# Kernel optimization log

Measured on AMD Instinct MI355X. Metric: run time of the kernel, lower is better.

The kernel has to match this reference:

```python
import jax, jax.numpy as jnp
import numpy as np
from jax import lax
import math

B, CH, BINS, CROP = 8, 2, 1024, 1024
NUM_BANDS = 4
FF = 2048
EPS = 1e-5
SCALE = 0.02  # weight init scale for numeric stability


def _inorm(x, g, b):
    # InstanceNorm2d: x [B, C, H, W], normalize over (H, W) per (B, C); biased var
    m = x.mean(axis=(2, 3), keepdims=True)
    v = x.var(axis=(2, 3), keepdims=True)
    return (x - m) / jnp.sqrt(v + EPS) * g[None, :, None, None] + b[None, :, None, None]


def _dwconv(x, k):
    # depthwise conv1d: x [B, bins, W], k [bins, 1, 3], padding=1, groups=bins
    return lax.conv_general_dilated(x, k, (1,), [(1, 1)],
                                    dimension_numbers=('NCH', 'OIH', 'NCH'),
                                    feature_group_count=x.shape[1])


def setup_inputs() -> dict:
    key = jax.random.key(0)
    ks = jax.random.split(key, 12)
    inp = {
        'x': jax.random.normal(ks[0], (B, CH, BINS, CROP), jnp.float32),
        'prev_qk': jax.random.normal(ks[1], (B, NUM_BANDS, CROP, CROP), jnp.float32),
        'g_in': jnp.ones((CROP,), jnp.float32),
        'b_in': jnp.zeros((CROP,), jnp.float32),
        'W_in': jax.random.normal(ks[2], (1, CH), jnp.float32) * SCALE,
        'bias_in': jnp.zeros((1,), jnp.float32),
        'g1': jnp.ones((CROP,), jnp.float32),
        'b1': jnp.zeros((CROP,), jnp.float32),
        'Wq': jax.random.normal(ks[3], (BINS, BINS), jnp.float32) * SCALE,
        'Wk': jax.random.normal(ks[4], (BINS, BINS), jnp.float32) * SCALE,
        'Wv': jax.random.normal(ks[5], (BINS, BINS), jnp.float32) * SCALE,
        'Wo': jax.random.normal(ks[6], (BINS, BINS), jnp.float32) * SCALE,
        'kq': jax.random.normal(ks[7], (BINS, 1, 3), jnp.float32) * SCALE,
        'kk': jax.random.normal(ks[8], (BINS, 1, 3), jnp.float32) * SCALE,
        'kv': jax.random.normal(ks[9], (BINS, 1, 3), jnp.float32) * SCALE,
        'pos_w': jax.random.normal(ks[10], (BINS // NUM_BANDS, CROP), jnp.float32) * SCALE,
        'g2': jnp.ones((CROP,), jnp.float32),
        'b2': jnp.zeros((CROP,), jnp.float32),
        'W_ff': jax.random.normal(ks[11], (1, 2), jnp.float32) * SCALE,
        'bias_ff': jnp.zeros((1,), jnp.float32),
        'W1': jax.random.normal(jax.random.fold_in(key, 100), (FF, BINS), jnp.float32) * SCALE,
        'W2': jax.random.normal(jax.random.fold_in(key, 101), (BINS, FF), jnp.float32) * SCALE,
    }
    return inp


def reference(x, prev_qk, g_in, b_in, W_in, bias_in, g1, b1, Wq, Wk, Wv, Wo,
              kq, kk, kv, pos_w, g2, b2, W_ff, bias_ff, W1, W2):
    b = x.shape[0]
    nb = NUM_BANDS
    hd = BINS // nb
    # in_norm + in_project: transposed layout [B, CROP, BINS, CH]
    xt = jnp.transpose(x, (0, 3, 2, 1))
    xt = _inorm(xt, g_in, b_in)
    xt = jnp.einsum('bwhc,oc->bwho', xt, W_in) + bias_in  # [B,CROP,BINS,1]
    x0 = jnp.transpose(xt, (0, 3, 2, 1))                  # [B,1,BINS,CROP]
    # norm1 + attention over frames (w == CROP, c == BINS)
    h = jnp.transpose(_inorm(jnp.transpose(x0, (0, 3, 2, 1)), g1, b1), (0, 3, 2, 1))
    a_in = jnp.transpose(h, (0, 3, 2, 1))[..., 0]         # [B, W, BINS]
    q = jnp.einsum('bwc,oc->bwo', a_in, Wq)
    q = jnp.transpose(_dwconv(jnp.transpose(q, (0, 2, 1)), kq), (0, 2, 1))
    k = jnp.einsum('bwc,oc->bwo', a_in, Wk)
    k = jnp.transpose(_dwconv(jnp.transpose(k, (0, 2, 1)), kk), (0, 2, 1))
    v = jnp.einsum('bwc,oc->bwo', a_in, Wv)
    v = jnp.transpose(_dwconv(jnp.transpose(v, (0, 2, 1)), kv), (0, 2, 1))
    q4 = jnp.transpose(q.reshape(b, CROP, nb, hd), (0, 2, 1, 3))   # [B,nb,W,hd]
    k4 = jnp.transpose(k.reshape(b, CROP, nb, hd), (0, 2, 3, 1))   # [B,nb,hd,W]
    v4 = jnp.transpose(v.reshape(b, CROP, nb, hd), (0, 2, 1, 3))   # [B,nb,W,hd]
    # relative-position bias via pad-and-shift
    p = jnp.matmul(q4, pos_w)                                      # [B,nb,W,CROP]
    p = jnp.pad(p, ((0, 0), (0, 0), (0, 0), (1, 0)))
    p = jnp.swapaxes(p, 2, 3)[:, :, 1:, :]                         # [B,nb,CROP,W]
    qk = (jnp.matmul(q4, k4) + p) / math.sqrt(BINS)
    qk = qk + prev_qk
    a = jax.nn.softmax(qk, axis=-1)
    o = jnp.transpose(jnp.matmul(a, v4), (0, 2, 1, 3)).reshape(b, CROP, BINS)
    o = jnp.einsum('bwc,oc->bwo', o, Wo)                           # [B,W,BINS]
    h4 = jnp.transpose(o[..., None], (0, 3, 2, 1))                 # [B,1,BINS,CROP]
    x1 = jnp.concatenate([x0, h4], axis=1)                         # [B,2,BINS,CROP]
    # norm2 + ff_project + squared-ReLU FFN
    hn = _inorm(jnp.transpose(x1, (0, 3, 2, 1)), g2, b2)           # [B,CROP,BINS,2]
    hn = jnp.einsum('bwhc,oc->bwho', hn, W_ff) + bias_ff           # [B,CROP,BINS,1]
    hn = jnp.transpose(hn, (0, 3, 2, 1))                           # [B,1,BINS,CROP]
    ht = jnp.swapaxes(hn, 2, 3)                                    # [B,1,CROP,BINS]
    ht = jnp.square(jax.nn.relu(jnp.einsum('bowc,fc->bowf', ht, W1)))
    ht = jnp.einsum('bowf,cf->bowc', ht, W2)
    hf = jnp.swapaxes(ht, 2, 3)                                    # [B,1,BINS,CROP]
    out = jnp.concatenate([x1, hf], axis=1)                        # [B,3,BINS,CROP]
    return out, qk
```

## Files before the change

### kernel.cpp

```cpp
#include <hip/hip_runtime.h>
#include <stdint.h>

#define DEVI __device__ __forceinline__

typedef __attribute__((ext_vector_type(8))) short bf16x8;
typedef __attribute__((ext_vector_type(4))) float f32x4;

#define B_    8
#define CROP_ 1024
#define BINS_ 1024
#define NB_   4
#define HD_   256
#define FF_   2048
#define EPSF  1e-5f
#define OUT0_ELEMS (8ull*3ull*1024ull*1024ull)
#define MBYTE (1024ull*1024ull)
#define M1ELEM (1024ll*1024ll)
#define SMCAP 8.0f

DEVI unsigned short f2bf(float f) {
  unsigned u = __builtin_bit_cast(unsigned, f);
  u += 0x7fffu + ((u >> 16) & 1u);
  return (unsigned short)(u >> 16);
}
DEVI float bf2f(unsigned short h) {
  unsigned u = ((unsigned)h) << 16;
  return __builtin_bit_cast(float, u);
}

DEVI void gload16(const unsigned short* g, unsigned short* l) {
  __builtin_amdgcn_global_load_lds(
      (const __attribute__((address_space(1))) unsigned int*)g,
      (__attribute__((address_space(3))) unsigned int*)l, 16, 0, 0);
}

__global__ __launch_bounds__(256) void k_conv_all(
    const float* __restrict__ Wq, const float* __restrict__ Wk,
    const float* __restrict__ Wv, const float* __restrict__ Wo,
    const float* __restrict__ W1, const float* __restrict__ W2,
    const float* __restrict__ pw,
    unsigned short* __restrict__ WQKVB, unsigned short* __restrict__ WOB,
    unsigned short* __restrict__ W1B, unsigned short* __restrict__ W2B,
    unsigned short* __restrict__ PWT) {
  long long i = (long long)blockIdx.x*256 + threadIdx.x;
  long long stride = (long long)gridDim.x*256;
  const long long total = 8*M1ELEM + (1 << 18);
  for (; i < total; i += stride) {
    if (i < 3*M1ELEM) {
      const float* s = i < M1ELEM ? Wq : (i < 2*M1ELEM ? Wk : Wv);
      WQKVB[i] = f2bf(s[i & (M1ELEM-1)]);
    } else if (i < 4*M1ELEM) { WOB[i-3*M1ELEM] = f2bf(Wo[i-3*M1ELEM]); }
    else if (i < 6*M1ELEM)   { W1B[i-4*M1ELEM] = f2bf(W1[i-4*M1ELEM]); }
    else if (i < 8*M1ELEM)   { W2B[i-6*M1ELEM] = f2bf(W2[i-6*M1ELEM]); }
    else {
      long long j = i - 8*M1ELEM;
      int w = (int)(j >> 8), d = (int)(j & 255);
      PWT[j] = f2bf(pw[d*1024 + w]);
    }
  }
}

__global__ __launch_bounds__(256) void k_instx0(const float* __restrict__ x,
    const float* __restrict__ g_in, const float* __restrict__ b_in,
    const float* __restrict__ W_in, const float* __restrict__ bias_in,
    float* __restrict__ outp, float* __restrict__ x0t) {
  int b = blockIdx.y, w0 = blockIdx.x*32;
  int t = threadIdx.x, wl = t & 31, p = t >> 5;
  const float* xb = x + (size_t)b*2*M1ELEM + w0 + wl;
  float s = 0.f, ss = 0.f;
  for (int i = p*256; i < p*256 + 256; ++i) {
    float v = xb[(size_t)i*CROP_];
    s += v; ss += v*v;
  }
  __shared__ float ls[8][32], lss[8][32];
  __shared__ float s_coef[32], s_add[32];
  ls[p][wl] = s; lss[p][wl] = ss;
  __syncthreads();
  float W0 = W_in[0], W1 = W_in[1], bi = bias_in[0];
  float sW = W0 + W1;
  if (t < 32) {
    float S = 0.f, SS = 0.f;
    for (int q = 0; q < 8; ++q) { S += ls[q][t]; SS += lss[q][t]; }
    float m = S*(1.f/2048.f);
    float var = SS*(1.f/2048.f) - m*m;
    float r = rsqrtf(var + EPSF);
    int w = w0 + t;
    float coef = r*g_in[w];
    s_coef[t] = coef;
    s_add[t] = b_in[w]*sW + bi - coef*m*sW;
  }
  __syncthreads();
  __shared__ float tile[32][33];
  int tx = wl, ty = p;
  float coef = s_coef[tx], add = s_add[tx];
  int w = w0 + tx;
  for (int h0 = 0; h0 < BINS_; h0 += 32) {
#pragma unroll
    for (int q = 0; q < 4; ++q) {
      int h = h0 + ty + q*8;
      size_t i0 = ((size_t)b*2*BINS_ + h)*CROP_ + w;
      float val = coef*(W0*x[i0] + W1*x[i0 + (size_t)M1ELEM]) + add;
      outp[(((size_t)b*3)*BINS_ + h)*CROP_ + w] = val;
      tile[ty + q*8][tx] = val;
    }
    __syncthreads();
#pragma unroll
    for (int q = 0; q < 4; ++q)
      x0t[((size_t)b*CROP_ + w0 + ty + q*8)*BINS_ + h0 + tx] = tile[tx][ty + q*8];
    __syncthreads();
  }
}

__global__ __launch_bounds__(256) void k_norm1(const float* __restrict__ x0t,
    const float* __restrict__ g1, const float* __restrict__ b1,
    unsigned short* __restrict__ ain) {
  int r = blockIdx.x;
  int w = r & (CROP_ - 1);
  int t = threadIdx.x;
  const float* row = x0t + (size_t)r*BINS_;
  float v[4], s = 0.f, ss = 0.f;
  for (int q = 0; q < 4; ++q) { v[q] = row[t + q*256]; s += v[q]; ss += v[q]*v[q]; }
  for (int off = 32; off; off >>= 1) { s += __shfl_xor(s, off); ss += __shfl_xor(ss, off); }
  __shared__ float red[8];
  int wv = t >> 6;
  if ((t & 63) == 0) { red[wv] = s; red[4 + wv] = ss; }
  __syncthreads();
  s = red[0] + red[1] + red[2] + red[3];
  ss = red[4] + red[5] + red[6] + red[7];
  float m = s*(1.f/1024.f);
  float var = ss*(1.f/1024.f) - m*m;
  float rs = rsqrtf(var + EPSF);
  float g = g1[w], bb = b1[w];
  for (int q = 0; q < 4; ++q)
    ain[(size_t)r*BINS_ + t + q*256] = f2bf((v[q] - m)*rs*g + bb);
}

__global__ __launch_bounds__(256) void k_norm2(const float* __restrict__ x0t,
    const float* __restrict__ o2,
    const float* __restrict__ g2, const float* __restrict__ b2,
    const float* __restrict__ W_ff, const float* __restrict__ bias_ff,
    unsigned short* __restrict__ hn) {
  int r = blockIdx.x;
  int w = r & (CROP_ - 1);
  int t = threadIdx.x;
  const float* ra = x0t + (size_t)r*BINS_;
  const float* rb = o2 + (size_t)r*BINS_;
  float va[4], vb[4], s = 0.f, ss = 0.f;
  for (int q = 0; q < 4; ++q) {
    va[q] = ra[t + q*256]; vb[q] = rb[t + q*256];
    s += va[q] + vb[q]; ss += va[q]*va[q] + vb[q]*vb[q];
  }
  for (int off = 32; off; off >>= 1) { s += __shfl_xor(s, off); ss += __shfl_xor(ss, off); }
  __shared__ float red[8];
  int wv = t >> 6;
  if ((t & 63) == 0) { red[wv] = s; red[4 + wv] = ss; }
  __syncthreads();
  s = red[0] + red[1] + red[2] + red[3];
  ss = red[4] + red[5] + red[6] + red[7];
  float m = s*(1.f/2048.f);
  float var = ss*(1.f/2048.f) - m*m;
  float rs = rsqrtf(var + EPSF);
  float W0 = W_ff[0], W1f = W_ff[1];
  float gg = g2[w]*rs;
  float add = b2[w]*(W0 + W1f) + bias_ff[0];
  for (int q = 0; q < 4; ++q)
    hn[(size_t)r*BINS_ + t + q*256] = f2bf(gg*(W0*(va[q] - m) + W1f*(vb[q] - m)) + add);
}

__global__ __launch_bounds__(256) void k_dwconv(const unsigned short* __restrict__ qkvb,
    const float* __restrict__ kq, const float* __restrict__ kk2,
    unsigned short* __restrict__ qkvc) {
  int w = blockIdx.x, b = blockIdx.y, which = blockIdx.z;
  int t = threadIdx.x;
  const float* kw = which == 0 ? kq : kk2;
  const unsigned short* r0 = qkvb + (size_t)which*8*M1ELEM + ((size_t)b*CROP_ + w)*BINS_;
  unsigned short* d0 = qkvc + (size_t)which*8*M1ELEM + ((size_t)b*CROP_ + w)*BINS_;
  for (int q = 0; q < 4; ++q) {
    int c = t + q*256;
    float k0 = kw[c*3], k1 = kw[c*3 + 1], k2 = kw[c*3 + 2];
    float acc = bf2f(r0[c]) * k1;
    if (w > 0)        acc += bf2f(r0[c - BINS_]) * k0;
    if (w < CROP_-1)  acc += bf2f(r0[c + BINS_]) * k2;
    d0[c] = f2bf(acc);
  }
}

__global__ __launch_bounds__(256) void k_dwconv_trV(const unsigned short* __restrict__ vb,
    const float* __restrict__ kv, unsigned short* __restrict__ vct) {
  int b = blockIdx.z;
  int w0 = blockIdx.x*32, c0 = blockIdx.y*32;
  int tx = threadIdx.x, ty = threadIdx.y;
  __shared__ unsigned short tile[34][33];
  const unsigned short* S = vb + (size_t)b*M1ELEM;
#pragma unroll
  for (int q = 0; q < 4; ++q) {
    int wl = ty + q*8;
    tile[wl + 1][tx] = S[(size_t)(w0 + wl)*BINS_ + c0 + tx];
  }
  if (ty == 0) tile[0][tx]  = (w0 > 0)          ? S[(size_t)(w0 - 1)*BINS_ + c0 + tx] : (unsigned short)0;
  if (ty == 1) tile[33][tx] = (w0 + 32 < CROP_) ? S[(size_t)(w0 + 32)*BINS_ + c0 + tx] : (unsigned short)0;
  __syncthreads();
  unsigned short* D = vct + (size_t)b*M1ELEM;
#pragma unroll
  for (int q = 0; q < 4; ++q) {
    int cl = ty + q*8;
    int c = c0 + cl;
    float k0 = kv[c*3], k1 = kv[c*3 + 1], k2 = kv[c*3 + 2];
    float val = k0*bf2f(tile[tx][cl]) + k1*bf2f(tile[tx + 1][cl]) + k2*bf2f(tile[tx + 2][cl]);
    D[(size_t)c*CROP_ + w0 + tx] = f2bf(val);
  }
}

#define BUFB 49152

template<int AC, int BC, int ABY>
DEVI void stage_gen(const unsigned short* Ab, int lda, const unsigned short* Bb, int ldb,
                    int k0, unsigned short* buf, int t, int wv) {
  int trow = t >> 3;
  int colel = ((t & 7) ^ (trow & 7)) << 3;
  unsigned short* lbase = buf + wv*512;
  const unsigned short* ga = Ab + (size_t)trow*lda + k0 + colel;
#pragma unroll
  for (int c = 0; c < AC; ++c)
    gload16(ga + (size_t)(c*64)*lda, lbase + c*4096);
  const unsigned short* gb = Bb + (size_t)trow*ldb + k0 + colel;
  unsigned short* lbb = buf + ABY/2 + wv*512;
#pragma unroll
  for (int c = 0; c < BC; ++c)
    gload16(gb + (size_t)(c*64)*ldb, lbb + c*4096);
}

template<int MODE>
__global__ __launch_bounds__(512) void k_gemm3(
    const unsigned short* __restrict__ A, int lda,
    const unsigned short* __restrict__ Bt, int ldb,
    void* __restrict__ C, int ldc, int K, float* __restrict__ C2, int ch)
{
  __shared__ __align__(16) unsigned short lds[3*24576];
  const unsigned short* Ab = A + (size_t)blockIdx.x*256*lda;
  const unsigned short* Bb = Bt + (size_t)blockIdx.y*128*ldb;
  const int t = threadIdx.x;
  const int wv = t >> 6, ln = t & 63;
  const int wm = wv >> 1, wn = wv & 1;
  const int lr = ln & 15, lk = ln >> 4;
  const int sx = (lr & 7) << 4;
  const int NT = K >> 6;
  stage_gen<4,2,32768>(Ab, lda, Bb, ldb, 0,   lds,           t, wv);
  stage_gen<4,2,32768>(Ab, lda, Bb, ldb, 64,  lds + 24576,   t, wv);
  stage_gen<4,2,32768>(Ab, lda, Bb, ldb, 128, lds + 49152,   t, wv);
  asm volatile("s_waitcnt vmcnt(12)" ::: "memory");
  __builtin_amdgcn_s_barrier();

  f32x4 acc[4][4] = {};
  for (int kt = 0; kt < NT; ++kt) {
    const int cur = kt % 3;
    const char* bufc = (const char*)lds + cur*BUFB;
    bf16x8 af[2][4], bf[2][4];
#pragma unroll
    for (int kk = 0; kk < 2; ++kk) {
#pragma unroll
      for (int mi = 0; mi < 4; ++mi) {
        int row = wm*64 + mi*16 + lr;
        af[kk][mi] = *(const bf16x8*)(bufc + ((row*128 + kk*64 + lk*16) ^ sx));
      }
#pragma unroll
      for (int ni = 0; ni < 4; ++ni) {
        int row = wn*64 + ni*16 + lr;
        bf[kk][ni] = *(const bf16x8*)(bufc + 32768 + ((row*128 + kk*64 + lk*16) ^ sx));
      }
    }
    asm volatile("s_waitcnt lgkmcnt(0)" ::: "memory");
    __builtin_amdgcn_s_barrier();
    if (kt + 3 < NT)
      stage_gen<4,2,32768>(Ab, lda, Bb, ldb, (kt+3)*64, (unsigned short*)((char*)lds + cur*BUFB), t, wv);
    __builtin_amdgcn_s_setprio(1);
#pragma unroll
    for (int kk = 0; kk < 2; ++kk)
#pragma unroll
      for (int mi = 0; mi < 4; ++mi)
#pragma unroll
        for (int ni = 0; ni < 4; ++ni)
          acc[mi][ni] = __builtin_amdgcn_mfma_f32_16x16x32_bf16(af[kk][mi], bf[kk][ni], acc[mi][ni], 0, 0, 0);
    __builtin_amdgcn_s_setprio(0);
    if (kt + 1 < NT) {
      int rem = (NT-1 < kt+3 ? NT-1 : kt+3) - (kt+1);
      if (rem >= 2)      asm volatile("s_waitcnt vmcnt(12)" ::: "memory");
      else if (rem == 1) asm volatile("s_waitcnt vmcnt(6)"  ::: "memory");
      else               asm volatile("s_waitcnt vmcnt(0)"  ::: "memory");
      __builtin_amdgcn_s_barrier();
    }
  }

  if (MODE != 3) {
    const int row0 = blockIdx.x*256 + wm*64 + lk*4;
    const int col0 = blockIdx.y*128 + wn*64 + lr;
#pragma unroll
    for (int mi = 0; mi < 4; ++mi)
#pragma unroll
      for (int ni = 0; ni < 4; ++ni)
#pragma unroll
        for (int j = 0; j < 4; ++j) {
          int row = row0 + mi*16 + j;
          int col = col0 + ni*16;
          float v = acc[mi][ni][j];
          if (MODE == 0 || MODE == 4) {
            ((float*)C)[(size_t)row*ldc + col] = v;
          } else if (MODE == 2) {
            float rr = fmaxf(v, 0.f);
            ((unsigned short*)C)[(size_t)row*ldc + col] = f2bf(rr*rr);
          } else if (MODE == 5) {
            ((unsigned short*)C)[(size_t)(col >> 10)*8*M1ELEM + (size_t)row*1024 + (col & 1023)] = f2bf(v);
          }
        }
  }
  if (MODE == 3 || MODE == 4) {
    __syncthreads();
    float* ldsT = (float*)lds + wv*4160;
#pragma unroll
    for (int mi = 0; mi < 4; ++mi)
#pragma unroll
      for (int ni = 0; ni < 4; ++ni)
#pragma unroll
        for (int j = 0; j < 4; ++j)
          ldsT[(ni*16 + lr)*65 + mi*16 + lk*4 + j] = acc[mi][ni][j];
    asm volatile("s_waitcnt lgkmcnt(0)" ::: "memory");
    int l16 = ln & 15, csub = ln >> 4;
    int b = blockIdx.x >> 2;
    int wbase = ((blockIdx.x & 3) << 8) + wm*64 + l16*4;
    float* outc = C2 + (((size_t)b*3 + ch)*BINS_)*CROP_;
#pragma unroll
    for (int cb = 0; cb < 16; ++cb) {
      int cl = cb*4 + csub;
      float4 v4;
      v4.x = ldsT[cl*65 + l16*4 + 0];
      v4.y = ldsT[cl*65 + l16*4 + 1];
      v4.z = ldsT[cl*65 + l16*4 + 2];
      v4.w = ldsT[cl*65 + l16*4 + 3];
      *(float4*)&outc[(size_t)(blockIdx.y*128 + wn*64 + cl)*CROP_ + wbase] = v4;
    }
  }
}

DEVI void stage_qk(const unsigned short* qc_b, const unsigned short* kc_b,
                   const unsigned short* pwt, int bx, int by, int k0,
                   unsigned short* buf, int t, int wv) {
  int trow = t >> 3;
  int colel = ((t & 7) ^ (trow & 7)) << 3;
  unsigned short* lbase = buf + wv*512;
  if (k0 < 256) {
    const unsigned short* ga = qc_b + (size_t)(bx*256 + trow)*BINS_ + k0 + colel;
#pragma unroll
    for (int c = 0; c < 4; ++c)
      gload16(ga + (size_t)(c*64)*BINS_, lbase + c*4096);
  } else {
    const unsigned short* ga = pwt + (size_t)(bx*256 + trow)*HD_ + (k0 - 256) + colel;
#pragma unroll
    for (int c = 0; c < 4; ++c)
      gload16(ga + (size_t)(c*64)*HD_, lbase + c*4096);
  }
  const unsigned short* gbsrc = (k0 < 256) ? kc_b : qc_b;
  int kb = (k0 < 256) ? k0 : k0 - 256;
  const unsigned short* gb = gbsrc + (size_t)(by*128 + trow)*BINS_ + kb + colel;
  unsigned short* lbb = buf + 16384 + wv*512;
#pragma unroll
  for (int c = 0; c < 2; ++c)
    gload16(gb + (size_t)(c*64)*BINS_, lbb + c*4096);
}

__global__ __launch_bounds__(512) void k_qkpos2(
    const unsigned short* __restrict__ qc, const unsigned short* __restrict__ kc,
    const unsigned short* __restrict__ pwt,
    const float* __restrict__ prev, float* __restrict__ qkout,
    unsigned short* __restrict__ Pbuf, float* __restrict__ Lg)
{
  __shared__ __align__(16) unsigned short lds[3*24576];
  const int z = blockIdx.z, b = z >> 2, n = z & 3;
  const size_t bandoff = (size_t)b*CROP_*BINS_ + (size_t)n*HD_;
  const unsigned short* qc_b = qc + bandoff;
  const unsigned short* kc_b = kc + bandoff;
  const int bx = blockIdx.x, by = blockIdx.y;
  const int t = threadIdx.x;
  const int wv = t >> 6, ln = t & 63;
  const int wm = wv >> 1, wn = wv & 1;
  const int lr = ln & 15, lk = ln >> 4;
  const int sx = (lr & 7) << 4;
  const int NT = 8;
  stage_qk(qc_b, kc_b, pwt, bx, by, 0,   lds,         t, wv);
  stage_qk(qc_b, kc_b, pwt, bx, by, 64,  lds + 24576, t, wv);
  stage_qk(qc_b, kc_b, pwt, bx, by, 128, lds + 49152, t, wv);
  asm volatile("s_waitcnt vmcnt(12)" ::: "memory");
  __builtin_amdgcn_s_barrier();

  f32x4 acc[4][4] = {};
  for (int kt = 0; kt < NT; ++kt) {
    const int cur = kt % 3;
    const char* bufc = (const char*)lds + cur*BUFB;
    bf16x8 af[2][4], bf[2][4];
#pragma unroll
    for (int kk = 0; kk < 2; ++kk) {
#pragma unroll
      for (int mi = 0; mi < 4; ++mi) {
        int row = wm*64 + mi*16 + lr;
        af[kk][mi] = *(const bf16x8*)(bufc + ((row*128 + kk*64 + lk*16) ^ sx));
      }
#pragma unroll
      for (int ni = 0; ni < 4; ++ni) {
        int row = wn*64 + ni*16 + lr;
        bf[kk][ni] = *(const bf16x8*)(bufc + 32768 + ((row*128 + kk*64 + lk*16) ^ sx));
      }
    }
    asm volatile("s_waitcnt lgkmcnt(0)" ::: "memory");
    __builtin_amdgcn_s_barrier();
    if (kt + 3 < NT)
      stage_qk(qc_b, kc_b, pwt, bx, by, (kt+3)*64, (unsigned short*)((char*)lds + cur*BUFB), t, wv);
    __builtin_amdgcn_s_setprio(1);
#pragma unroll
    for (int kk = 0; kk < 2; ++kk)
#pragma unroll
      for (int mi = 0; mi < 4; ++mi)
#pragma unroll
        for (int ni = 0; ni < 4; ++ni)
          acc[mi][ni] = __builtin_amdgcn_mfma_f32_16x16x32_bf16(af[kk][mi], bf[kk][ni], acc[mi][ni], 0, 0, 0);
    __builtin_amdgcn_s_setprio(0);
    if (kt + 1 < NT) {
      int rem = (NT-1 < kt+3 ? NT-1 : kt+3) - (kt+1);
      if (rem >= 2)      asm volatile("s_waitcnt vmcnt(12)" ::: "memory");
      else if (rem == 1) asm volatile("s_waitcnt vmcnt(6)"  ::: "memory");
      else               asm volatile("s_waitcnt vmcnt(0)"  ::: "memory");
      __builtin_amdgcn_s_barrier();
    }
  }

  const float* pz = prev + (size_t)z*M1ELEM;
  float* oz = qkout + (size_t)z*M1ELEM;
  unsigned short* Pz = Pbuf + (size_t)z*M1ELEM;
  const int row0g = bx*256;
  const int col0 = by*128 + wn*64 + lr;
  float* slf = (float*)lds;
  const int rbase = wm*64 + lk*4;
#pragma unroll
  for (int mi = 0; mi < 4; ++mi) {
    float psum[4] = {0.f, 0.f, 0.f, 0.f};
#pragma unroll
    for (int ni = 0; ni < 4; ++ni)
#pragma unroll
      for (int j = 0; j < 4; ++j) {
        size_t idx = (size_t)(row0g + rbase + mi*16 + j)*CROP_ + col0 + ni*16;
        float val = acc[mi][ni][j]*0.03125f + pz[idx];
        oz[idx] = val;
        float p = __expf(val - SMCAP);
        Pz[idx] = f2bf(p);
        psum[j] += p;
      }
#pragma unroll
    for (int off = 1; off < 16; off <<= 1)
#pragma unroll
      for (int j = 0; j < 4; ++j) psum[j] += __shfl_xor(psum[j], off);
    if (lr == 0)
#pragma unroll
      for (int j = 0; j < 4; ++j) slf[wn*256 + rbase + mi*16 + j] = psum[j];
  }
  __syncthreads();
  if (t < 256) {
    size_t si = ((size_t)z*CROP_ + row0g + t)*8 + by;
    Lg[si] = slf[t] + slf[256 + t];
  }
}

__global__ __launch_bounds__(512) void k_pv3(
    const unsigned short* __restrict__ P, const float* __restrict__ Lg,
    const unsigned short* __restrict__ vct, unsigned short* __restrict__ ob)
{
  __shared__ __align__(16) unsigned short lds[3*24576];
  __shared__ float s_il[128];
  const int z = blockIdx.y, b = z >> 2, band = z & 3;
  const int bx = blockIdx.x;
  const unsigned short* Ab = P + (size_t)z*M1ELEM + (size_t)bx*128*CROP_;
  const unsigned short* Bb = vct + ((size_t)b*CROP_ + band*HD_)*CROP_;
  const int t = threadIdx.x;
  const int wv = t >> 6, ln = t & 63;
  const int wm = wv >> 2, wn = wv & 3;
  const int lr = ln & 15, lk = ln >> 4;
  const int sx = (lr & 7) << 4;
  const int NT = 16;
  if (t < 128) {
    size_t rg = (size_t)z*CROP_ + bx*128 + t;
    float l = 0.f;
#pragma unroll
    for (int cb = 0; cb < 8; ++cb) l += Lg[rg*8 + cb];
    s_il[t] = 1.f / l;
  }
  stage_gen<2,4,16384>(Ab, CROP_, Bb, CROP_, 0,   lds,         t, wv);
  stage_gen<2,4,16384>(Ab, CROP_, Bb, CROP_, 64,  lds + 24576, t, wv);
  stage_gen<2,4,16384>(Ab, CROP_, Bb, CROP_, 128, lds + 49152, t, wv);
  asm volatile("s_waitcnt vmcnt(12) lgkmcnt(0)" ::: "memory");
  __builtin_amdgcn_s_barrier();

  f32x4 acc[4][4] = {};
  for (int kt = 0; kt < NT; ++kt) {
    const int cur = kt % 3;
    const char* bufc = (const char*)lds + cur*BUFB;
    bf16x8 af[2][4], bf[2][4];
#pragma unroll
    for (int kk = 0; kk < 2; ++kk) {
#pragma unroll
      for (int mi = 0; mi < 4; ++mi) {
        int row = wm*64 + mi*16 + lr;
        af[kk][mi] = *(const bf16x8*)(bufc + ((row*128 + kk*64 + lk*16) ^ sx));
      }
#pragma unroll
      for (int ni = 0; ni < 4; ++ni) {
        int row = wn*64 + ni*16 + lr;
        bf[kk][ni] = *(const bf16x8*)(bufc + 16384 + ((row*128 + kk*64 + lk*16) ^ sx));
      }
    }
    asm volatile("s_waitcnt lgkmcnt(0)" ::: "memory");
    __builtin_amdgcn_s_barrier();
    if (kt + 3 < NT)
      stage_gen<2,4,16384>(Ab, CROP_, Bb, CROP_, (kt+3)*64, (unsigned short*)((char*)lds + cur*BUFB), t, wv);
    __builtin_amdgcn_s_setprio(1);
#pragma unroll
    for (int kk = 0; kk < 2; ++kk)
#pragma unroll
      for (int mi = 0; mi < 4; ++mi)
#pragma unroll
        for (int ni = 0; ni < 4; ++ni)
          acc[mi][ni] = __builtin_amdgcn_mfma_f32_16x16x32_bf16(af[kk][mi], bf[kk][ni], acc[mi][ni], 0, 0, 0);
    __builtin_amdgcn_s_setprio(0);
    if (kt + 1 < NT) {
      int rem = (NT-1 < kt+3 ? NT-1 : kt+3) - (kt+1);
      if (rem >= 2)      asm volatile("s_waitcnt vmcnt(12)" ::: "memory");
      else if (rem == 1) asm volatile("s_waitcnt vmcnt(6)"  ::: "memory");
      else               asm volatile("s_waitcnt vmcnt(0)"  ::: "memory");
      __builtin_amdgcn_s_barrier();
    }
  }
#pragma unroll
  for (int mi = 0; mi < 4; ++mi)
#pragma unroll
    for (int j = 0; j < 4; ++j) {
      int rl = wm*64 + mi*16 + lk*4 + j;
      float il = s_il[rl];
#pragma unroll
      for (int ni = 0; ni < 4; ++ni) {
        int col = band*HD_ + wn*64 + ni*16 + lr;
        ob[((size_t)b*CROP_ + bx*128 + rl)*BINS_ + col] = f2bf(acc[mi][ni][j]*il);
      }
    }
}

extern "C" void kernel_launch(void* const* d_in, const int* in_sizes, int n_in,
                              void* d_out, int out_size, void* d_ws, size_t ws_size,
                              hipStream_t stream) {
  (void)in_sizes; (void)n_in; (void)out_size; (void)ws_size;
  const float* x       = (const float*)d_in[0];
  const float* prev_qk = (const float*)d_in[1];
  const float* g_in    = (const float*)d_in[2];
  const float* b_in    = (const float*)d_in[3];
  const float* W_in    = (const float*)d_in[4];
  const float* bias_in = (const float*)d_in[5];
  const float* g1      = (const float*)d_in[6];
  const float* b1      = (const float*)d_in[7];
  const float* Wq      = (const float*)d_in[8];
  const float* Wk      = (const float*)d_in[9];
  const float* Wv      = (const float*)d_in[10];
  const float* Wo      = (const float*)d_in[11];
  const float* kq      = (const float*)d_in[12];
  const float* kk      = (const float*)d_in[13];
  const float* kv      = (const float*)d_in[14];
  const float* pos_w   = (const float*)d_in[15];
  const float* g2      = (const float*)d_in[16];
  const float* b2      = (const float*)d_in[17];
  const float* W_ff    = (const float*)d_in[18];
  const float* bias_ff = (const float*)d_in[19];
  const float* W1      = (const float*)d_in[20];
  const float* W2      = (const float*)d_in[21];

  char* ws = (char*)d_ws;
  unsigned short* WQKVB = (unsigned short*)(ws + 0*MBYTE);
  unsigned short* WOB   = (unsigned short*)(ws + 6*MBYTE);
  unsigned short* W1B   = (unsigned short*)(ws + 8*MBYTE);
  unsigned short* W2B   = (unsigned short*)(ws + 12*MBYTE);
  unsigned short* PWT   = (unsigned short*)(ws + 16*MBYTE);
  float*          Lg    = (float*)(ws + 17*MBYTE);
  float*          X0T   = (float*)(ws + 20*MBYTE);
  unsigned short* AIN   = (unsigned short*)(ws + 52*MBYTE);
  unsigned short* QKVB  = (unsigned short*)(ws + 68*MBYTE);
  unsigned short* PBUF  = (unsigned short*)(ws + 52*MBYTE);
  unsigned short* QKVC  = (unsigned short*)(ws + 116*MBYTE);
  float*          O2    = (float*)(ws + 116*MBYTE);
  unsigned short* OB    = (unsigned short*)(ws + 148*MBYTE);
  unsigned short* VCT   = (unsigned short*)(ws + 164*MBYTE);
  unsigned short* HN    = (unsigned short*)(ws + 52*MBYTE);
  unsigned short* HT    = (unsigned short*)(ws + 20*MBYTE);

  float* outp  = (float*)d_out;
  float* qkout = outp + OUT0_ELEMS;

  dim3 blk256(256, 1, 1);
  dim3 blk512(512, 1, 1);
  dim3 blk32x8(32, 8, 1);

  k_conv_all<<<8448, blk256, 0, stream>>>(Wq, Wk, Wv, Wo, W1, W2, pos_w,
                                          WQKVB, WOB, W1B, W2B, PWT);
  k_instx0<<<dim3(32, 8, 1), blk256, 0, stream>>>(x, g_in, b_in, W_in, bias_in, outp, X0T);
  k_norm1<<<8192, blk256, 0, stream>>>(X0T, g1, b1, AIN);
  k_gemm3<5><<<dim3(32, 24, 1), blk512, 0, stream>>>(AIN, 1024, WQKVB, 1024, QKVB, 0, 1024, nullptr, 0);
  k_dwconv<<<dim3(1024, 8, 2), blk256, 0, stream>>>(QKVB, kq, kk, QKVC);
  k_dwconv_trV<<<dim3(32, 32, 8), blk32x8, 0, stream>>>(QKVB + (size_t)2*8*M1ELEM, kv, VCT);
  k_qkpos2<<<dim3(4, 8, 32), blk512, 0, stream>>>(QKVC, QKVC + (size_t)8*M1ELEM, PWT,
                                                  prev_qk, qkout, PBUF, Lg);
  k_pv3<<<dim3(8, 32, 1), blk512, 0, stream>>>(PBUF, Lg, VCT, OB);
  k_gemm3<4><<<dim3(32, 8, 1), blk512, 0, stream>>>(OB, 1024, WOB, 1024, O2, 1024, 1024, outp, 1);
  k_norm2<<<8192, blk256, 0, stream>>>(X0T, O2, g2, b2, W_ff, bias_ff, HN);
  k_gemm3<2><<<dim3(32, 16, 1), blk512, 0, stream>>>(HN, 1024, W1B, 1024, HT, 2048, 1024, nullptr, 0);
  k_gemm3<3><<<dim3(32, 8, 1), blk512, 0, stream>>>(HT, 2048, W2B, 2048, nullptr, 1024, 2048, outp, 2);
}
```

Before: 462.8 us.

## Split LDS fragment loads to overlap MFMA and add XCD-aware block swizzle

The GEMM inner loop now loads the first k-half of the A/B fragments, waits only for those, and issues their MFMAs while the second-half LDS reads are still in flight. The barrier and the next global-to-LDS prefetch are moved between the two MFMA halves. Separately, every GEMM kernel remaps its flat block index so that consecutive tiles land on the same XCD, which is meant to improve L2 reuse of shared A/B rows. This adds sched_barriers and index arithmetic, and the relaxed lgkmcnt wait relies on LDS reads completing in issue order.

```diff
diff --git a/kernel.cpp b/kernel.cpp
--- a/kernel.cpp
+++ b/kernel.cpp
@@ -32,6 +32,16 @@
   __builtin_amdgcn_global_load_lds(
       (const __attribute__((address_space(1))) unsigned int*)g,
       (__attribute__((address_space(3))) unsigned int*)l, 16, 0, 0);
+}
+
+DEVI void xcdswz(int& bx, int& by, int& bz) {
+  int gx = gridDim.x, gy = gridDim.y;
+  int nwg = gx*gy*gridDim.z;
+  int flat = blockIdx.x + gx*(blockIdx.y + gy*blockIdx.z);
+  int s = (flat & 7)*(nwg >> 3) + (flat >> 3);
+  bx = s % gx; s /= gx;
+  by = s % gy;
+  bz = s / gy;
 }
 
 __global__ __launch_bounds__(256) void k_conv_all(
@@ -230,6 +240,57 @@
     gload16(gb + (size_t)(c*64)*ldb, lbb + c*4096);
 }
 
+#define RING_BODY(BOFF, ...)                                                           \
+    bf16x8 af[2][4], bf[2][4];                                                         \
+    _Pragma("unroll")                                                                  \
+    for (int mi = 0; mi < 4; ++mi) {                                                   \
+      int row = wm*64 + mi*16 + lr;                                                    \
+      af[0][mi] = *(const bf16x8*)(bufc + ((row*128 + lk*16) ^ sx));                   \
+    }                                                                                  \
+    _Pragma("unroll")                                                                  \
+    for (int ni = 0; ni < 4; ++ni) {                                                   \
+      int row = wn*64 + ni*16 + lr;                                                    \
+      bf[0][ni] = *(const bf16x8*)(bufc + BOFF + ((row*128 + lk*16) ^ sx));            \
+    }                                                                                  \
+    __builtin_amdgcn_sched_barrier(0);                                                 \
+    _Pragma("unroll")                                                                  \
+    for (int mi = 0; mi < 4; ++mi) {                                                   \
+      int row = wm*64 + mi*16 + lr;                                                    \
+      af[1][mi] = *(const bf16x8*)(bufc + ((row*128 + 64 + lk*16) ^ sx));              \
+    }                                                                                  \
+    _Pragma("unroll")                                                                  \
+    for (int ni = 0; ni < 4; ++ni) {                                                   \
+      int row = wn*64 + ni*16 + lr;                                                    \
+      bf[1][ni] = *(const bf16x8*)(bufc + BOFF + ((row*128 + 64 + lk*16) ^ sx));       \
+    }                                                                                  \
+    asm volatile("s_waitcnt lgkmcnt(8)" ::: "memory");                                 \
+    __builtin_amdgcn_sched_barrier(0);                                                 \
+    __builtin_amdgcn_s_setprio(1);                                                     \
+    _Pragma("unroll")                                                                  \
+    for (int mi = 0; mi < 4; ++mi)                                                     \
+      _Pragma("unroll")                                                                \
+      for (int ni = 0; ni < 4; ++ni)                                                   \
+        acc[mi][ni] = __builtin_amdgcn_mfma_f32_16x16x32_bf16(af[0][mi], bf[0][ni], acc[mi][ni], 0, 0, 0); \
+    __builtin_amdgcn_s_setprio(0);                                                     \
+    __builtin_amdgcn_sched_barrier(0);                                                 \
+    asm volatile("s_waitcnt lgkmcnt(0)" ::: "memory");                                 \
+    __builtin_amdgcn_s_barrier();                                                      \
+    __VA_ARGS__;                                                                       \
+    __builtin_amdgcn_s_setprio(1);                                                     \
+    _Pragma("unroll")                                                                  \
+    for (int mi = 0; mi < 4; ++mi)                                                     \
+      _Pragma("unroll")                                                                \
+      for (int ni = 0; ni < 4; ++ni)                                                   \
+        acc[mi][ni] = __builtin_amdgcn_mfma_f32_16x16x32_bf16(af[1][mi], bf[1][ni], acc[mi][ni], 0, 0, 0); \
+    __builtin_amdgcn_s_setprio(0);                                                     \
+    if (kt + 1 < NT) {                                                                 \
+      int rem = (NT-1 < kt+3 ? NT-1 : kt+3) - (kt+1);                                  \
+      if (rem >= 2)      asm volatile("s_waitcnt vmcnt(12)" ::: "memory");             \
+      else if (rem == 1) asm volatile("s_waitcnt vmcnt(6)"  ::: "memory");             \
+      else               asm volatile("s_waitcnt vmcnt(0)"  ::: "memory");             \
+      __builtin_amdgcn_s_barrier();                                                    \
+    }
+
 template<int MODE>
 __global__ __launch_bounds__(512) void k_gemm3(
     const unsigned short* __restrict__ A, int lda,
@@ -237,8 +298,11 @@
     void* __restrict__ C, int ldc, int K, float* __restrict__ C2, int ch)
 {
   __shared__ __align__(16) unsigned short lds[3*24576];
-  const unsigned short* Ab = A + (size_t)blockIdx.x*256*lda;
-  const unsigned short* Bb = Bt + (size_t)blockIdx.y*128*ldb;
+  int bxs, bys, bzs;
+  xcdswz(bxs, bys, bzs);
+  (void)bzs;
+  const unsigned short* Ab = A + (size_t)bxs*256*lda;
+  const unsigned short* Bb = Bt + (size_t)bys*128*ldb;
   const int t = threadIdx.x;
   const int wv = t >> 6, ln = t & 63;
   const int wm = wv >> 1, wn = wv & 1;
@@ -255,45 +319,14 @@
   for (int kt = 0; kt < NT; ++kt) {
     const int cur = kt % 3;
     const char* bufc = (const char*)lds + cur*BUFB;
-    bf16x8 af[2][4], bf[2][4];
-#pragma unroll
-    for (int kk = 0; kk < 2; ++kk) {
-#pragma unroll
-      for (int mi = 0; mi < 4; ++mi) {
-        int row = wm*64 + mi*16 + lr;
-        af[kk][mi] = *(const bf16x8*)(bufc + ((row*128 + kk*64 + lk*16) ^ sx));
-      }
-#pragma unroll
-      for (int ni = 0; ni < 4; ++ni) {
-        int row = wn*64 + ni*16 + lr;
-        bf[kk][ni] = *(const bf16x8*)(bufc + 32768 + ((row*128 + kk*64 + lk*16) ^ sx));
-      }
-    }
-    asm volatile("s_waitcnt lgkmcnt(0)" ::: "memory");
-    __builtin_amdgcn_s_barrier();
-    if (kt + 3 < NT)
-      stage_gen<4,2,32768>(Ab, lda, Bb, ldb, (kt+3)*64, (unsigned short*)((char*)lds + cur*BUFB), t, wv);
-    __builtin_amdgcn_s_setprio(1);
-#pragma unroll
-    for (int kk = 0; kk < 2; ++kk)
-#pragma unroll
-      for (int mi = 0; mi < 4; ++mi)
-#pragma unroll
-        for (int ni = 0; ni < 4; ++ni)
-          acc[mi][ni] = __builtin_amdgcn_mfma_f32_16x16x32_bf16(af[kk][mi], bf[kk][ni], acc[mi][ni], 0, 0, 0);
-    __builtin_amdgcn_s_setprio(0);
-    if (kt + 1 < NT) {
-      int rem = (NT-1 < kt+3 ? NT-1 : kt+3) - (kt+1);
-      if (rem >= 2)      asm volatile("s_waitcnt vmcnt(12)" ::: "memory");
-      else if (rem == 1) asm volatile("s_waitcnt vmcnt(6)"  ::: "memory");
-      else               asm volatile("s_waitcnt vmcnt(0)"  ::: "memory");
-      __builtin_amdgcn_s_barrier();
-    }
+    RING_BODY(32768,
+      if (kt + 3 < NT) stage_gen<4,2,32768>(Ab, lda, Bb, ldb, (kt+3)*64,
+                                            (unsigned short*)((char*)lds + cur*BUFB), t, wv))
   }
 
   if (MODE != 3) {
-    const int row0 = blockIdx.x*256 + wm*64 + lk*4;
-    const int col0 = blockIdx.y*128 + wn*64 + lr;
+    const int row0 = bxs*256 + wm*64 + lk*4;
+    const int col0 = bys*128 + wn*64 + lr;
 #pragma unroll
     for (int mi = 0; mi < 4; ++mi)
 #pragma unroll
@@ -325,8 +358,8 @@
           ldsT[(ni*16 + lr)*65 + mi*16 + lk*4 + j] = acc[mi][ni][j];
     asm volatile("s_waitcnt lgkmcnt(0)" ::: "memory");
     int l16 = ln & 15, csub = ln >> 4;
-    int b = blockIdx.x >> 2;
-    int wbase = ((blockIdx.x & 3) << 8) + wm*64 + l16*4;
+    int b = bxs >> 2;
+    int wbase = ((bxs & 3) << 8) + wm*64 + l16*4;
     float* outc = C2 + (((size_t)b*3 + ch)*BINS_)*CROP_;
 #pragma unroll
     for (int cb = 0; cb < 16; ++cb) {
@@ -336,7 +369,7 @@
       v4.y = ldsT[cl*65 + l16*4 + 1];
       v4.z = ldsT[cl*65 + l16*4 + 2];
       v4.w = ldsT[cl*65 + l16*4 + 3];
-      *(float4*)&outc[(size_t)(blockIdx.y*128 + wn*64 + cl)*CROP_ + wbase] = v4;
+      *(float4*)&outc[(size_t)(bys*128 + wn*64 + cl)*CROP_ + wbase] = v4;
     }
   }
 }
@@ -374,11 +407,12 @@
     unsigned short* __restrict__ Pbuf, float* __restrict__ Lg)
 {
   __shared__ __align__(16) unsigned short lds[3*24576];
-  const int z = blockIdx.z, b = z >> 2, n = z & 3;
+  int bx, by, z;
+  xcdswz(bx, by, z);
+  const int b = z >> 2, n = z & 3;
   const size_t bandoff = (size_t)b*CROP_*BINS_ + (size_t)n*HD_;
   const unsigned short* qc_b = qc + bandoff;
   const unsigned short* kc_b = kc + bandoff;
-  const int bx = blockIdx.x, by = blockIdx.y;
   const int t = threadIdx.x;
   const int wv = t >> 6, ln = t & 63;
   const int wm = wv >> 1, wn = wv & 1;
@@ -395,40 +429,9 @@
   for (int kt = 0; kt < NT; ++kt) {
     const int cur = kt % 3;
     const char* bufc = (const char*)lds + cur*BUFB;
-    bf16x8 af[2][4], bf[2][4];
-#pragma unroll
-    for (int kk = 0; kk < 2; ++kk) {
-#pragma unroll
-      for (int mi = 0; mi < 4; ++mi) {
-        int row = wm*64 + mi*16 + lr;
-        af[kk][mi] = *(const bf16x8*)(bufc + ((row*128 + kk*64 + lk*16) ^ sx));
-      }
-#pragma unroll
-      for (int ni = 0; ni < 4; ++ni) {
-        int row = wn*64 + ni*16 + lr;
-        bf[kk][ni] = *(const bf16x8*)(bufc + 32768 + ((row*128 + kk*64 + lk*16) ^ sx));
-      }
-    }
-    asm volatile("s_waitcnt lgkmcnt(0)" ::: "memory");
-    __builtin_amdgcn_s_barrier();
-    if (kt + 3 < NT)
-      stage_qk(qc_b, kc_b, pwt, bx, by, (kt+3)*64, (unsigned short*)((char*)lds + cur*BUFB), t, wv);
-    __builtin_amdgcn_s_setprio(1);
-#pragma unroll
-    for (int kk = 0; kk < 2; ++kk)
-#pragma unroll
-      for (int mi = 0; mi < 4; ++mi)
-#pragma unroll
-        for (int ni = 0; ni < 4; ++ni)
-          acc[mi][ni] = __builtin_amdgcn_mfma_f32_16x16x32_bf16(af[kk][mi], bf[kk][ni], acc[mi][ni], 0, 0, 0);
-    __builtin_amdgcn_s_setprio(0);
-    if (kt + 1 < NT) {
-      int rem = (NT-1 < kt+3 ? NT-1 : kt+3) - (kt+1);
-      if (rem >= 2)      asm volatile("s_waitcnt vmcnt(12)" ::: "memory");
-      else if (rem == 1) asm volatile("s_waitcnt vmcnt(6)"  ::: "memory");
-      else               asm volatile("s_waitcnt vmcnt(0)"  ::: "memory");
-      __builtin_amdgcn_s_barrier();
-    }
+    RING_BODY(32768,
+      if (kt + 3 < NT) stage_qk(qc_b, kc_b, pwt, bx, by, (kt+3)*64,
+                                (unsigned short*)((char*)lds + cur*BUFB), t, wv))
   }
 
   const float* pz = prev + (size_t)z*M1ELEM;
@@ -473,8 +476,10 @@
 {
   __shared__ __align__(16) unsigned short lds[3*24576];
   __shared__ float s_il[128];
-  const int z = blockIdx.y, b = z >> 2, band = z & 3;
-  const int bx = blockIdx.x;
+  int bx, z, zz;
+  xcdswz(bx, z, zz);
+  (void)zz;
+  const int b = z >> 2, band = z & 3;
   const unsigned short* Ab = P + (size_t)z*M1ELEM + (size_t)bx*128*CROP_;
   const unsigned short* Bb = vct + ((size_t)b*CROP_ + band*HD_)*CROP_;
   const int t = threadIdx.x;
@@ -500,40 +505,9 @@
   for (int kt = 0; kt < NT; ++kt) {
     const int cur = kt % 3;
     const char* bufc = (const char*)lds + cur*BUFB;
-    bf16x8 af[2][4], bf[2][4];
-#pragma unroll
-    for (int kk = 0; kk < 2; ++kk) {
-#pragma unroll
-      for (int mi = 0; mi < 4; ++mi) {
-        int row = wm*64 + mi*16 + lr;
-        af[kk][mi] = *(const bf16x8*)(bufc + ((row*128 + kk*64 + lk*16) ^ sx));
-      }
-#pragma unroll
-      for (int ni = 0; ni < 4; ++ni) {
-        int row = wn*64 + ni*16 + lr;
-        bf[kk][ni] = *(const bf16x8*)(bufc + 16384 + ((row*128 + kk*64 + lk*16) ^ sx));
-      }
-    }
-    asm volatile("s_waitcnt lgkmcnt(0)" ::: "memory");
-    __builtin_amdgcn_s_barrier();
-    if (kt + 3 < NT)
-      stage_gen<2,4,16384>(Ab, CROP_, Bb, CROP_, (kt+3)*64, (unsigned short*)((char*)lds + cur*BUFB), t, wv);
-    __builtin_amdgcn_s_setprio(1);
-#pragma unroll
-    for (int kk = 0; kk < 2; ++kk)
-#pragma unroll
-      for (int mi = 0; mi < 4; ++mi)
-#pragma unroll
-        for (int ni = 0; ni < 4; ++ni)
-          acc[mi][ni] = __builtin_amdgcn_mfma_f32_16x16x32_bf16(af[kk][mi], bf[kk][ni], acc[mi][ni], 0, 0, 0);
-    __builtin_amdgcn_s_setprio(0);
-    if (kt + 1 < NT) {
-      int rem = (NT-1 < kt+3 ? NT-1 : kt+3) - (kt+1);
-      if (rem >= 2)      asm volatile("s_waitcnt vmcnt(12)" ::: "memory");
-      else if (rem == 1) asm volatile("s_waitcnt vmcnt(6)"  ::: "memory");
-      else               asm volatile("s_waitcnt vmcnt(0)"  ::: "memory");
-      __builtin_amdgcn_s_barrier();
-    }
+    RING_BODY(16384,
+      if (kt + 3 < NT) stage_gen<2,4,16384>(Ab, CROP_, Bb, CROP_, (kt+3)*64,
+                                            (unsigned short*)((char*)lds + cur*BUFB), t, wv))
   }
 #pragma unroll
   for (int mi = 0; mi < 4; ++mi)
```

Measured after the change: 469.0 us. Within noise of the previous version (+1.3%).
